# Optimization experiments

Measured on AMD Instinct MI355X. Metric: run time of the kernel, lower is better.

The kernel has to match this reference:

```python
import jax, jax.numpy as jnp
import numpy as np

TOP_K = 8


def setup_inputs() -> dict:
    key = jax.random.key(0)
    k1, k2 = jax.random.split(key)
    hidden_states = jax.random.normal(k1, (16384, 2048), dtype=jnp.float32)
    weight = jax.random.normal(k2, (64, 2048), dtype=jnp.float32) * 0.02
    return {"hidden_states": hidden_states, "weight": weight}


def reference(hidden_states, weight):
    # router_logits = F.linear(hidden_states, weight): [T, E]
    router_logits = jnp.einsum('th,eh->te', hidden_states, weight)
    # softmax in float32 as in the original
    router_probs = jax.nn.softmax(router_logits.astype(jnp.float32), axis=-1)
    router_top_values, router_indices = jax.lax.top_k(router_probs, TOP_K)
    # norm_topk_prob=True: renormalize selected probs to sum to 1
    router_top_values = router_top_values / jnp.sum(router_top_values, axis=-1, keepdims=True)
    return (router_logits,
            router_top_values.astype(hidden_states.dtype),
            router_indices)
```

## Files before the change

### kernel.cpp

```cpp
#include <hip/hip_runtime.h>
#include <math.h>

#define T_TOKENS 16384
#define HID      2048
#define NE       64
#define TOPK     8
#define TM       32
#define BK       128
#define NCH      (HID / BK)
#define RSTR     272
#define A_SPL    (TM * RSTR)
#define ABUF     (3 * A_SPL)
#define LDS_BYTES (2 * ABUF)

#define WS_B_BYTES  786432
#define WS_LG_OFF   786432
#define WS_NEEDED   (WS_LG_OFF + (size_t)T_TOKENS * NE * 8)

typedef float    f32x4  __attribute__((ext_vector_type(4)));
typedef short    short8 __attribute__((ext_vector_type(8)));
typedef unsigned uint4v __attribute__((ext_vector_type(4)));

#define MFMA16(A, B, C) __builtin_amdgcn_mfma_f32_16x16x32_bf16((A), (B), (C), 0, 0, 0)

static __device__ __forceinline__ unsigned short f2bf(float x) {
    unsigned u = __builtin_bit_cast(unsigned, x);
    return (unsigned short)((u + 0x7FFFu + ((u >> 16) & 1u)) >> 16);
}

static __device__ __forceinline__ void split8(const float4 v0, const float4 v1,
                                              uint4v& p0, uint4v& p1, uint4v& p2)
{
    const float x[8] = {v0.x, v0.y, v0.z, v0.w, v1.x, v1.y, v1.z, v1.w};
    #pragma unroll
    for (int j = 0; j < 4; ++j) {
        const float xe = x[2 * j], xo = x[2 * j + 1];
        const unsigned ue  = __builtin_bit_cast(unsigned, xe);
        const unsigned m0e = (ue + 0x8000u) & 0xFFFF0000u;
        const float    r1e = xe - __builtin_bit_cast(float, m0e);
        const unsigned u1e = __builtin_bit_cast(unsigned, r1e);
        const unsigned m1e = (u1e + 0x8000u) & 0xFFFF0000u;
        const float    r2e = r1e - __builtin_bit_cast(float, m1e);
        const unsigned u2e = __builtin_bit_cast(unsigned, r2e);
        const unsigned uo  = __builtin_bit_cast(unsigned, xo);
        const unsigned m0o = (uo + 0x8000u) & 0xFFFF0000u;
        const float    r1o = xo - __builtin_bit_cast(float, m0o);
        const unsigned u1o = __builtin_bit_cast(unsigned, r1o);
        const unsigned m1o = (u1o + 0x8000u) & 0xFFFF0000u;
        const float    r2o = r1o - __builtin_bit_cast(float, m1o);
        const unsigned u2o = __builtin_bit_cast(unsigned, r2o);
        p0[j] = m0o | (m0e >> 16);
        p1[j] = m1o | (m1e >> 16);
        p2[j] = (u2o & 0xFFFF0000u) | (u2e >> 16);
    }
}

__global__ __launch_bounds__(256) void split_weight_kernel(
    const float* __restrict__ weight, uint4v* __restrict__ ws)
{
    const int n = blockIdx.x;
    const int o = threadIdx.x;
    const float4 w0 = *(const float4*)&weight[(size_t)n * HID + o * 8];
    const float4 w1 = *(const float4*)&weight[(size_t)n * HID + o * 8 + 4];
    uint4v p0, p1, p2;
    split8(w0, w1, p0, p1, p2);
    const int t    = o >> 2;
    const int lane = (o & 3) * 16 + (n & 15);
    const int e    = n >> 4;
    const int base = t * 256 + e * 64 + lane;
    ws[base]         = p0;
    ws[base + 16384] = p1;
    ws[base + 32768] = p2;
}

template<bool FUSED>
__global__ __launch_bounds__(256, 2) void router_kernel(
    const float* __restrict__ hidden,
    const short8* __restrict__ bfrag,
    double* __restrict__ lgws,
    float* __restrict__ out_logits,
    float* __restrict__ out_vals,
    float* __restrict__ out_idxf)
{
    __shared__ __align__(16) char smem[LDS_BYTES];
    double (*lg)[NE + 1] = reinterpret_cast<double(*)[NE + 1]>(smem);

    const int tid  = threadIdx.x;
    const int tok0 = blockIdx.x * TM;
    const int lane = tid & 63;
    const int wave = tid >> 6;

    const int fr = lane & 15;
    const int fk = lane >> 4;

    int rowmap[4], colmap[4];
    {
        const unsigned short mb = f2bf((float)fr);
        const unsigned short ob = f2bf(0.03125f);
        short8 vm, vo;
        #pragma unroll
        for (int j = 0; j < 8; ++j) { vm[j] = (short)mb; vo[j] = (short)ob; }
        const f32x4 z = {0.f, 0.f, 0.f, 0.f};
        const f32x4 pr = MFMA16(vm, vo, z);
        const f32x4 pc = MFMA16(vo, vm, z);
        #pragma unroll
        for (int i = 0; i < 4; ++i) {
            rowmap[i] = (int)(pr[i] + 0.5f);
            colmap[i] = (int)(pc[i] + 0.5f);
        }
    }

    const int ar   = tid >> 3;
    const int ac16 = (tid & 7) * 16;
    const float* aG = hidden + (size_t)(tok0 + ar) * HID + ac16;
    const int aWOff = ar * RSTR + ac16 * 2;

    const short8* bP = bfrag + wave * 64 + lane;

    const int aOff0 = fr * RSTR + fk * 16;
    const int aOff1 = (16 + fr) * RSTR + fk * 16;

    const f32x4 z4 = {0.f, 0.f, 0.f, 0.f};
    f32x4 acch[2] = {z4, z4};
    f32x4 accl[2] = {z4, z4};
    double accd[2][4] = {{0, 0, 0, 0}, {0, 0, 0, 0}};

    float4 pa[4];
    short8 Bcur0, Bcur1, Bcur2;
    short8 Bnx0, Bnx1, Bnx2;

    {
        #pragma unroll
        for (int q = 0; q < 4; ++q) pa[q] = *(const float4*)(aG + 4 * q);
        uint4v p0, p1, p2;
        char* aW = smem + aWOff;
        split8(pa[0], pa[1], p0, p1, p2);
        *(uint4v*)(aW            ) = p0;
        *(uint4v*)(aW +   A_SPL  ) = p1;
        *(uint4v*)(aW + 2*A_SPL  ) = p2;
        split8(pa[2], pa[3], p0, p1, p2);
        *(uint4v*)(aW             + 16) = p0;
        *(uint4v*)(aW +   A_SPL   + 16) = p1;
        *(uint4v*)(aW + 2*A_SPL   + 16) = p2;
    }
    Bcur0 = bP[0];
    Bcur1 = bP[16384];
    Bcur2 = bP[32768];
    Bnx0  = bP[256];
    Bnx1  = bP[256 + 16384];
    Bnx2  = bP[256 + 32768];
    __syncthreads();

    for (int c = 0; c < NCH; ++c) {
        const char* bufc = smem + (c & 1) * ABUF;

        short8 A00 = *(const short8*)(bufc + aOff0);
        short8 A01 = *(const short8*)(bufc + A_SPL + aOff0);
        short8 A02 = *(const short8*)(bufc + 2 * A_SPL + aOff0);
        short8 A10 = *(const short8*)(bufc + aOff1);
        short8 A11 = *(const short8*)(bufc + A_SPL + aOff1);
        short8 A12 = *(const short8*)(bufc + 2 * A_SPL + aOff1);

        if (c + 1 < NCH) {
            const int off = (c + 1) * BK;
            #pragma unroll
            for (int q = 0; q < 4; ++q) pa[q] = *(const float4*)(aG + off + 4 * q);
        }

        #pragma unroll
        for (int st = 0; st < 4; ++st) {
            short8 An00, An01, An02, An10, An11, An12;
            if (st < 3) {
                const int ao = (st + 1) * 64;
                An00 = *(const short8*)(bufc + aOff0 + ao);
                An01 = *(const short8*)(bufc + A_SPL + aOff0 + ao);
                An02 = *(const short8*)(bufc + 2 * A_SPL + aOff0 + ao);
                An10 = *(const short8*)(bufc + aOff1 + ao);
                An11 = *(const short8*)(bufc + A_SPL + aOff1 + ao);
                An12 = *(const short8*)(bufc + 2 * A_SPL + aOff1 + ao);
            }
            short8 B20 = Bnx0, B21 = Bnx1, B22 = Bnx2;
            if (c < NCH - 1 || st < 2) {
                const int t2 = (c * 4 + st + 2) * 256;
                B20 = bP[t2];
                B21 = bP[t2 + 16384];
                B22 = bP[t2 + 32768];
            }

            acch[0] = MFMA16(A00, Bcur0, acch[0]);
            accl[0] = MFMA16(A00, Bcur1, accl[0]);
            accl[0] = MFMA16(A01, Bcur0, accl[0]);
            accl[0] = MFMA16(A01, Bcur1, accl[0]);
            accl[0] = MFMA16(A00, Bcur2, accl[0]);
            accl[0] = MFMA16(A02, Bcur0, accl[0]);
            acch[1] = MFMA16(A10, Bcur0, acch[1]);
            accl[1] = MFMA16(A10, Bcur1, accl[1]);
            accl[1] = MFMA16(A11, Bcur0, accl[1]);
            accl[1] = MFMA16(A11, Bcur1, accl[1]);
            accl[1] = MFMA16(A10, Bcur2, accl[1]);
            accl[1] = MFMA16(A12, Bcur0, accl[1]);

            if (st < 3) {
                A00 = An00; A01 = An01; A02 = An02;
                A10 = An10; A11 = An11; A12 = An12;
            }
            Bcur0 = Bnx0; Bcur1 = Bnx1; Bcur2 = Bnx2;
            Bnx0  = B20;  Bnx1  = B21;  Bnx2  = B22;
        }

        #pragma unroll
        for (int f = 0; f < 2; ++f) {
            #pragma unroll
            for (int i = 0; i < 4; ++i) accd[f][i] += (double)acch[f][i];
            acch[f] = z4;
        }

        if (c + 1 < NCH) {
            uint4v p0, p1, p2;
            char* aW = smem + ((c & 1) ^ 1) * ABUF + aWOff;
            split8(pa[0], pa[1], p0, p1, p2);
            *(uint4v*)(aW            ) = p0;
            *(uint4v*)(aW +   A_SPL  ) = p1;
            *(uint4v*)(aW + 2*A_SPL  ) = p2;
            split8(pa[2], pa[3], p0, p1, p2);
            *(uint4v*)(aW             + 16) = p0;
            *(uint4v*)(aW +   A_SPL   + 16) = p1;
            *(uint4v*)(aW + 2*A_SPL   + 16) = p2;
        }
        __syncthreads();
    }

    if constexpr (!FUSED) {
        #pragma unroll
        for (int f = 0; f < 2; ++f) {
            #pragma unroll
            for (int i = 0; i < 4; ++i) {
                const int trow = f * 16 + rowmap[i];
                const int tok  = tok0 + trow;
                const int e0   = wave * 16 + colmap[i];
                const double l0 = accd[f][i] + (double)accl[f][i];
                out_logits[(size_t)tok * NE + e0] = (float)l0;
                lgws[(size_t)tok * NE + e0]       = l0;
            }
        }
    } else {
        #pragma unroll
        for (int f = 0; f < 2; ++f) {
            #pragma unroll
            for (int i = 0; i < 4; ++i) {
                const int trow = f * 16 + rowmap[i];
                const int tok  = tok0 + trow;
                const int e0   = wave * 16 + colmap[i];
                const double l0 = accd[f][i] + (double)accl[f][i];
                out_logits[(size_t)tok * NE + e0] = (float)l0;
                lg[trow][e0] = l0;
            }
        }
        __syncthreads();

        for (int tt = wave; tt < TM; tt += 4) {
            double cur = lg[tt][lane];
            double first = 0.0;
            float  s = 0.f, myv = 0.f;
            int myi = 0;
            #pragma unroll
            for (int i = 0; i < TOPK; ++i) {
                double mv = cur;
                #pragma unroll
                for (int off = 32; off; off >>= 1) {
                    const double ov = __shfl_xor(mv, off);
                    mv = ov > mv ? ov : mv;
                }
                const unsigned long long m = __ballot(cur == mv);
                const int mi = __ffsll(m) - 1;
                if (i == 0) first = mv;
                const float e = expf((float)(mv - first));
                s += e;
                if (lane == i)  { myv = e; myi = mi; }
                if (lane == mi) cur = -INFINITY;
            }
            if (lane < TOPK) {
                const int tok = tok0 + tt;
                out_vals[(size_t)tok * TOPK + lane] = myv / s;
                out_idxf[(size_t)tok * TOPK + lane] = (float)myi;
            }
        }
    }
}

__global__ __launch_bounds__(256) void topk_kernel(
    const double* __restrict__ lgws,
    float* __restrict__ out_vals,
    float* __restrict__ out_idxf)
{
    const int lane = threadIdx.x & 63;
    const int gw   = (blockIdx.x * 256 + threadIdx.x) >> 6;
    for (int tok = gw; tok < T_TOKENS; tok += 4096) {
        double cur = lgws[(size_t)tok * NE + lane];
        double first = 0.0;
        float  s = 0.f, myv = 0.f;
        int myi = 0;
        #pragma unroll
        for (int i = 0; i < TOPK; ++i) {
            double mv = cur;
            #pragma unroll
            for (int off = 32; off; off >>= 1) {
                const double ov = __shfl_xor(mv, off);
                mv = ov > mv ? ov : mv;
            }
            const unsigned long long m = __ballot(cur == mv);
            const int mi = __ffsll(m) - 1;
            if (i == 0) first = mv;
            const float e = expf((float)(mv - first));
            s += e;
            if (lane == i)  { myv = e; myi = mi; }
            if (lane == mi) cur = -INFINITY;
        }
        if (lane < TOPK) {
            out_vals[(size_t)tok * TOPK + lane] = myv / s;
            out_idxf[(size_t)tok * TOPK + lane] = (float)myi;
        }
    }
}

extern "C" void kernel_launch(void* const* d_in, const int* in_sizes, int n_in,
                              void* d_out, int out_size, void* d_ws, size_t ws_size,
                              hipStream_t stream) {
    const float* hidden = (const float*)d_in[0];
    const float* weight = (const float*)d_in[1];

    float* out        = (float*)d_out;
    float* out_logits = out;
    float* out_vals   = out + (size_t)T_TOKENS * NE;
    float* out_idxf   = out + (size_t)T_TOKENS * NE + (size_t)T_TOKENS * TOPK;

    uint4v* ws   = (uint4v*)d_ws;
    double* lgws = (double*)((char*)d_ws + WS_LG_OFF);

    hipLaunchKernelGGL(split_weight_kernel, dim3(NE), dim3(256), 0, stream,
                       weight, ws);

    if (ws_size >= WS_NEEDED) {
        hipLaunchKernelGGL((router_kernel<false>), dim3(T_TOKENS / TM), dim3(256),
                           0, stream, hidden, (const short8*)ws, lgws,
                           out_logits, out_vals, out_idxf);
        hipLaunchKernelGGL(topk_kernel, dim3(1024), dim3(256), 0, stream,
                           lgws, out_vals, out_idxf);
    } else {
        hipLaunchKernelGGL((router_kernel<true>), dim3(T_TOKENS / TM), dim3(256),
                           0, stream, hidden, (const short8*)ws, (double*)nullptr,
                           out_logits, out_vals, out_idxf);
    }
}
```

Baseline: 219.2 us.

## Switch router GEMM to 32x32 MFMA with split-K across wave pairs

Replaces the 16x16x32 bf16 MFMA tiling, where each wave owned 16 experts over all 32 tokens, with 32x32x16 MFMAs. Waves now split two ways over experts and two ways over the K dimension, so each wave does half the K loop. The partial sums are combined through LDS at the end, and the weight fragment layout is rewritten to match. The aim is fewer MFMA issues and fewer A-fragment LDS reads per flop. In exchange it drops the software prefetch of the B and A fragments, adds an LDS reduction plus barrier, and leaves half the waves idle during the logit write.

```diff
diff --git a/kernel.cpp b/kernel.cpp
--- a/kernel.cpp
+++ b/kernel.cpp
@@ -13,15 +13,15 @@
 #define ABUF     (3 * A_SPL)
 #define LDS_BYTES (2 * ABUF)
 
-#define WS_B_BYTES  786432
 #define WS_LG_OFF   786432
 #define WS_NEEDED   (WS_LG_OFF + (size_t)T_TOKENS * NE * 8)
 
 typedef float    f32x4  __attribute__((ext_vector_type(4)));
+typedef float    f32x16 __attribute__((ext_vector_type(16)));
 typedef short    short8 __attribute__((ext_vector_type(8)));
 typedef unsigned uint4v __attribute__((ext_vector_type(4)));
 
-#define MFMA16(A, B, C) __builtin_amdgcn_mfma_f32_16x16x32_bf16((A), (B), (C), 0, 0, 0)
+#define MFMA32(A, B, C) __builtin_amdgcn_mfma_f32_32x32x16_bf16((A), (B), (C), 0, 0, 0)
 
 static __device__ __forceinline__ unsigned short f2bf(float x) {
     unsigned u = __builtin_bit_cast(unsigned, x);
@@ -64,13 +64,11 @@
     const float4 w1 = *(const float4*)&weight[(size_t)n * HID + o * 8 + 4];
     uint4v p0, p1, p2;
     split8(w0, w1, p0, p1, p2);
-    const int t    = o >> 2;
-    const int lane = (o & 3) * 16 + (n & 15);
-    const int e    = n >> 4;
-    const int base = t * 256 + e * 64 + lane;
-    ws[base]         = p0;
-    ws[base + 16384] = p1;
-    ws[base + 32768] = p2;
+    const int t   = o >> 1;
+    const int idx = t * 128 + (n >> 5) * 64 + (o & 1) * 32 + (n & 31);
+    ws[idx]         = p0;
+    ws[idx + 16384] = p1;
+    ws[idx + 32768] = p2;
 }
 
 template<bool FUSED>
@@ -83,83 +81,49 @@
     float* __restrict__ out_idxf)
 {
     __shared__ __align__(16) char smem[LDS_BYTES];
-    double (*lg)[NE + 1] = reinterpret_cast<double(*)[NE + 1]>(smem);
 
     const int tid  = threadIdx.x;
     const int tok0 = blockIdx.x * TM;
     const int lane = tid & 63;
     const int wave = tid >> 6;
-
-    const int fr = lane & 15;
-    const int fk = lane >> 4;
-
-    int rowmap[4], colmap[4];
-    {
-        const unsigned short mb = f2bf((float)fr);
-        const unsigned short ob = f2bf(0.03125f);
-        short8 vm, vo;
-        #pragma unroll
-        for (int j = 0; j < 8; ++j) { vm[j] = (short)mb; vo[j] = (short)ob; }
-        const f32x4 z = {0.f, 0.f, 0.f, 0.f};
-        const f32x4 pr = MFMA16(vm, vo, z);
-        const f32x4 pc = MFMA16(vo, vm, z);
-        #pragma unroll
-        for (int i = 0; i < 4; ++i) {
-            rowmap[i] = (int)(pr[i] + 0.5f);
-            colmap[i] = (int)(pc[i] + 0.5f);
-        }
-    }
+    const int eh   = wave & 1;
+    const int kh   = wave >> 1;
 
     const int ar   = tid >> 3;
     const int ac16 = (tid & 7) * 16;
     const float* aG = hidden + (size_t)(tok0 + ar) * HID + ac16;
     const int aWOff = ar * RSTR + ac16 * 2;
 
-    const short8* bP = bfrag + wave * 64 + lane;
-
-    const int aOff0 = fr * RSTR + fk * 16;
-    const int aOff1 = (16 + fr) * RSTR + fk * 16;
-
-    const f32x4 z4 = {0.f, 0.f, 0.f, 0.f};
-    f32x4 acch[2] = {z4, z4};
-    f32x4 accl[2] = {z4, z4};
-    double accd[2][4] = {{0, 0, 0, 0}, {0, 0, 0, 0}};
+    const int aOff = (lane & 31) * RSTR + (lane >> 5) * 16 + kh * 128;
+    const short8* bP = bfrag + eh * 64 + lane;
+
+    f32x16 acch, accl;
+    double accd[16];
+    #pragma unroll
+    for (int i = 0; i < 16; ++i) { acch[i] = 0.f; accl[i] = 0.f; accd[i] = 0.0; }
 
     float4 pa[4];
-    short8 Bcur0, Bcur1, Bcur2;
-    short8 Bnx0, Bnx1, Bnx2;
-
-    {
-        #pragma unroll
-        for (int q = 0; q < 4; ++q) pa[q] = *(const float4*)(aG + 4 * q);
-        uint4v p0, p1, p2;
-        char* aW = smem + aWOff;
-        split8(pa[0], pa[1], p0, p1, p2);
-        *(uint4v*)(aW            ) = p0;
-        *(uint4v*)(aW +   A_SPL  ) = p1;
-        *(uint4v*)(aW + 2*A_SPL  ) = p2;
-        split8(pa[2], pa[3], p0, p1, p2);
-        *(uint4v*)(aW             + 16) = p0;
-        *(uint4v*)(aW +   A_SPL   + 16) = p1;
-        *(uint4v*)(aW + 2*A_SPL   + 16) = p2;
-    }
-    Bcur0 = bP[0];
-    Bcur1 = bP[16384];
-    Bcur2 = bP[32768];
-    Bnx0  = bP[256];
-    Bnx1  = bP[256 + 16384];
-    Bnx2  = bP[256 + 32768];
+
+#define STAGE_A(dstbase) do {                                                     \
+    uint4v p0_, p1_, p2_;                                                         \
+    char* aW_ = (dstbase) + aWOff;                                                \
+    split8(pa[0], pa[1], p0_, p1_, p2_);                                          \
+    *(uint4v*)(aW_            ) = p0_;                                            \
+    *(uint4v*)(aW_ +   A_SPL  ) = p1_;                                            \
+    *(uint4v*)(aW_ + 2*A_SPL  ) = p2_;                                            \
+    split8(pa[2], pa[3], p0_, p1_, p2_);                                          \
+    *(uint4v*)(aW_             + 16) = p0_;                                       \
+    *(uint4v*)(aW_ +   A_SPL   + 16) = p1_;                                       \
+    *(uint4v*)(aW_ + 2*A_SPL   + 16) = p2_;                                       \
+} while (0)
+
+    #pragma unroll
+    for (int q = 0; q < 4; ++q) pa[q] = *(const float4*)(aG + 4 * q);
+    STAGE_A(smem);
     __syncthreads();
 
     for (int c = 0; c < NCH; ++c) {
         const char* bufc = smem + (c & 1) * ABUF;
-
-        short8 A00 = *(const short8*)(bufc + aOff0);
-        short8 A01 = *(const short8*)(bufc + A_SPL + aOff0);
-        short8 A02 = *(const short8*)(bufc + 2 * A_SPL + aOff0);
-        short8 A10 = *(const short8*)(bufc + aOff1);
-        short8 A11 = *(const short8*)(bufc + A_SPL + aOff1);
-        short8 A12 = *(const short8*)(bufc + 2 * A_SPL + aOff1);
 
         if (c + 1 < NCH) {
             const int off = (c + 1) * BK;
@@ -169,95 +133,80 @@
 
         #pragma unroll
         for (int st = 0; st < 4; ++st) {
-            short8 An00, An01, An02, An10, An11, An12;
-            if (st < 3) {
-                const int ao = (st + 1) * 64;
-                An00 = *(const short8*)(bufc + aOff0 + ao);
-                An01 = *(const short8*)(bufc + A_SPL + aOff0 + ao);
-                An02 = *(const short8*)(bufc + 2 * A_SPL + aOff0 + ao);
-                An10 = *(const short8*)(bufc + aOff1 + ao);
-                An11 = *(const short8*)(bufc + A_SPL + aOff1 + ao);
-                An12 = *(const short8*)(bufc + 2 * A_SPL + aOff1 + ao);
-            }
-            short8 B20 = Bnx0, B21 = Bnx1, B22 = Bnx2;
-            if (c < NCH - 1 || st < 2) {
-                const int t2 = (c * 4 + st + 2) * 256;
-                B20 = bP[t2];
-                B21 = bP[t2 + 16384];
-                B22 = bP[t2 + 32768];
-            }
-
-            acch[0] = MFMA16(A00, Bcur0, acch[0]);
-            accl[0] = MFMA16(A00, Bcur1, accl[0]);
-            accl[0] = MFMA16(A01, Bcur0, accl[0]);
-            accl[0] = MFMA16(A01, Bcur1, accl[0]);
-            accl[0] = MFMA16(A00, Bcur2, accl[0]);
-            accl[0] = MFMA16(A02, Bcur0, accl[0]);
-            acch[1] = MFMA16(A10, Bcur0, acch[1]);
-            accl[1] = MFMA16(A10, Bcur1, accl[1]);
-            accl[1] = MFMA16(A11, Bcur0, accl[1]);
-            accl[1] = MFMA16(A11, Bcur1, accl[1]);
-            accl[1] = MFMA16(A10, Bcur2, accl[1]);
-            accl[1] = MFMA16(A12, Bcur0, accl[1]);
-
-            if (st < 3) {
-                A00 = An00; A01 = An01; A02 = An02;
-                A10 = An10; A11 = An11; A12 = An12;
-            }
-            Bcur0 = Bnx0; Bcur1 = Bnx1; Bcur2 = Bnx2;
-            Bnx0  = B20;  Bnx1  = B21;  Bnx2  = B22;
-        }
-
-        #pragma unroll
-        for (int f = 0; f < 2; ++f) {
-            #pragma unroll
-            for (int i = 0; i < 4; ++i) accd[f][i] += (double)acch[f][i];
-            acch[f] = z4;
-        }
+            const char* ab = bufc + aOff + st * 32;
+            const short8 A0 = *(const short8*)(ab);
+            const short8 A1 = *(const short8*)(ab + A_SPL);
+            const short8 A2 = *(const short8*)(ab + 2 * A_SPL);
+            const int T = (c * 8 + kh * 4 + st) * 128;
+            const short8 B0 = bP[T];
+            const short8 B1 = bP[T + 16384];
+            const short8 B2 = bP[T + 32768];
+            acch = MFMA32(A0, B0, acch);
+            accl = MFMA32(A0, B1, accl);
+            accl = MFMA32(A1, B0, accl);
+            accl = MFMA32(A1, B1, accl);
+            accl = MFMA32(A0, B2, accl);
+            accl = MFMA32(A2, B0, accl);
+        }
+
+        #pragma unroll
+        for (int i = 0; i < 16; ++i) accd[i] += (double)acch[i];
+        #pragma unroll
+        for (int i = 0; i < 16; ++i) acch[i] = 0.f;
 
         if (c + 1 < NCH) {
-            uint4v p0, p1, p2;
-            char* aW = smem + ((c & 1) ^ 1) * ABUF + aWOff;
-            split8(pa[0], pa[1], p0, p1, p2);
-            *(uint4v*)(aW            ) = p0;
-            *(uint4v*)(aW +   A_SPL  ) = p1;
-            *(uint4v*)(aW + 2*A_SPL  ) = p2;
-            split8(pa[2], pa[3], p0, p1, p2);
-            *(uint4v*)(aW             + 16) = p0;
-            *(uint4v*)(aW +   A_SPL   + 16) = p1;
-            *(uint4v*)(aW + 2*A_SPL   + 16) = p2;
+            STAGE_A(smem + ((c & 1) ^ 1) * ABUF);
         }
         __syncthreads();
     }
 
-    if constexpr (!FUSED) {
-        #pragma unroll
-        for (int f = 0; f < 2; ++f) {
-            #pragma unroll
-            for (int i = 0; i < 4; ++i) {
-                const int trow = f * 16 + rowmap[i];
-                const int tok  = tok0 + trow;
-                const int e0   = wave * 16 + colmap[i];
-                const double l0 = accd[f][i] + (double)accl[f][i];
-                out_logits[(size_t)tok * NE + e0] = (float)l0;
-                lgws[(size_t)tok * NE + e0]       = l0;
-            }
-        }
-    } else {
-        #pragma unroll
-        for (int f = 0; f < 2; ++f) {
-            #pragma unroll
-            for (int i = 0; i < 4; ++i) {
-                const int trow = f * 16 + rowmap[i];
-                const int tok  = tok0 + trow;
-                const int e0   = wave * 16 + colmap[i];
-                const double l0 = accd[f][i] + (double)accl[f][i];
-                out_logits[(size_t)tok * NE + e0] = (float)l0;
-                lg[trow][e0] = l0;
-            }
-        }
+    int rowmap[16], colmap[16];
+    {
+        const unsigned short mb = f2bf((float)(lane & 31));
+        const unsigned short ob = f2bf(0.0625f);
+        short8 vm, vo;
+        #pragma unroll
+        for (int j = 0; j < 8; ++j) { vm[j] = (short)mb; vo[j] = (short)ob; }
+        f32x16 z;
+        #pragma unroll
+        for (int i = 0; i < 16; ++i) z[i] = 0.f;
+        const f32x16 pr = MFMA32(vm, vo, z);
+        const f32x16 pc = MFMA32(vo, vm, z);
+        #pragma unroll
+        for (int i = 0; i < 16; ++i) {
+            rowmap[i] = (int)(pr[i] + 0.5f);
+            colmap[i] = (int)(pc[i] + 0.5f);
+        }
+    }
+
+    double lfin[16];
+    #pragma unroll
+    for (int i = 0; i < 16; ++i) lfin[i] = accd[i] + (double)accl[i];
+
+    double* red = (double*)smem;
+    if (kh == 1) {
+        #pragma unroll
+        for (int i = 0; i < 16; ++i) red[(eh * 64 + lane) * 17 + i] = lfin[i];
+    }
+    __syncthreads();
+
+    double (*lg)[NE + 1] = reinterpret_cast<double(*)[NE + 1]>(smem + 17408);
+
+    if (kh == 0) {
+        #pragma unroll
+        for (int i = 0; i < 16; ++i) {
+            lfin[i] += red[(eh * 64 + lane) * 17 + i];
+            const int trow = rowmap[i];
+            const int tok  = tok0 + trow;
+            const int col  = eh * 32 + colmap[i];
+            out_logits[(size_t)tok * NE + col] = (float)lfin[i];
+            if constexpr (!FUSED) lgws[(size_t)tok * NE + col] = lfin[i];
+            else                  lg[trow][col] = lfin[i];
+        }
+    }
+
+    if constexpr (FUSED) {
         __syncthreads();
-
         for (int tt = wave; tt < TM; tt += 4) {
             double cur = lg[tt][lane];
             double first = 0.0;
```

After: 233.1 us. 6.3% more time.
